# Kernel tuning notes

Measured on AMD Instinct MI355X. Metric: run time of the kernel, lower is better.

The kernel has to match this reference:

```python
import jax, jax.numpy as jnp
import numpy as np

N = 8192
IN_F = 512
OUT_F = 64
ALPHA = 0.2  # LeakyReLU negative slope
NEG_INF = -9e15


def setup_inputs() -> dict:
    key = jax.random.key(0)
    k1, k2, k3, k4 = jax.random.split(key, 4)
    # xavier_uniform-style scale (gain=1.414)
    w_bound = 1.414 * np.sqrt(6.0 / (IN_F + OUT_F))
    a_bound = 1.414 * np.sqrt(6.0 / (2 * OUT_F + 1))
    return {
        "input": jax.random.normal(k1, (N, IN_F), dtype=jnp.float32),
        "adj": jax.random.randint(k2, (N, N), 0, 2, dtype=jnp.int32),
        "W": jax.random.uniform(k3, (IN_F, OUT_F), jnp.float32, -w_bound, w_bound),
        "a": jax.random.uniform(k4, (2 * OUT_F, 1), jnp.float32, -a_bound, a_bound),
        "sig_sample_size": 512,
    }


def reference(input, adj, W, a, sig_sample_size):
    h = input @ W  # [N, F]
    # Split 'a' so e_ij = leakyrelu(a1.h_i + a2.h_j) without the N*N*2F repeat/cat
    a1, a2 = a[:OUT_F, 0], a[OUT_F:, 0]  # [F], [F]
    e = jax.nn.leaky_relu((h @ a1)[:, None] + (h @ a2)[None, :], negative_slope=ALPHA)  # [N, N]
    attention = jnp.where(adj > 0, e, NEG_INF)
    attention = jax.nn.softmax(attention, axis=1)
    sig_scores = jnp.sum(attention, axis=0)  # [N]
    _, indices = jax.lax.top_k(sig_scores, sig_sample_size)
    return indices
```

## Files before the change

kernel.cpp:

```cpp
#include <hip/hip_runtime.h>
#include <stdint.h>

#define NROW 8192
#define IN_F 512
#define OUT_F 64
#define ALPHA 0.2f

__device__ float g_wa1[IN_F];
__device__ float g_wa2[IN_F];
__device__ float g_f1[NROW];
__device__ float g_f2[NROW];
__device__ float g_zinv[NROW];
__device__ double g_colsum[NROW];
__device__ unsigned long long g_mask[(size_t)NROW * 128];

__global__ void prep_wa(const float* __restrict__ W, const float* __restrict__ a) {
    int k = threadIdx.x;
    if (k < IN_F) {
        double s1 = 0.0, s2 = 0.0;
        for (int t = 0; t < OUT_F; ++t) {
            double w = (double)W[k * OUT_F + t];
            s1 += w * (double)a[t];
            s2 += w * (double)a[OUT_F + t];
        }
        g_wa1[k] = (float)s1;
        g_wa2[k] = (float)s2;
        #pragma unroll
        for (int i = 0; i < 16; ++i) g_colsum[k * 16 + i] = 0.0;
    }
}

__global__ void __launch_bounds__(256) compute_f(const float* __restrict__ in) {
    int wave = threadIdx.x >> 6, lane = threadIdx.x & 63;
    int row = blockIdx.x * 4 + wave;
    const float4* in4  = (const float4*)(in + (size_t)row * IN_F);
    const float4* wa14 = (const float4*)g_wa1;
    const float4* wa24 = (const float4*)g_wa2;
    double s1 = 0.0, s2 = 0.0;
    #pragma unroll
    for (int half = 0; half < 2; ++half) {
        int idx = half * 64 + lane;
        float4 x = in4[idx];
        float4 u = wa14[idx];
        float4 v = wa24[idx];
        s1 += (double)x.x*u.x + (double)x.y*u.y + (double)x.z*u.z + (double)x.w*u.w;
        s2 += (double)x.x*v.x + (double)x.y*v.y + (double)x.z*v.z + (double)x.w*v.w;
    }
    #pragma unroll
    for (int off = 32; off > 0; off >>= 1) {
        s1 += __shfl_down(s1, off, 64);
        s2 += __shfl_down(s2, off, 64);
    }
    if (lane == 0) { g_f1[row] = (float)s1; g_f2[row] = (float)s2; }
}

__global__ void __launch_bounds__(256) row_z_mask(const int* __restrict__ adj) {
    __shared__ float f2s[NROW];
    __shared__ double zpart[16];
    int tid = threadIdx.x;
    int wave = tid >> 6, lane = tid & 63;
    for (int k = tid; k < NROW / 4; k += 256)
        ((float4*)f2s)[k] = ((const float4*)g_f2)[k];
    __syncthreads();
    int row0 = blockIdx.x * 4;
    for (int r = 0; r < 4; ++r) {
        int row = row0 + r;
        float f1r = g_f1[row];
        const int4* arow = (const int4*)(adj + (size_t)row * NROW) + wave * 512;
        unsigned long long myword = 0;
        double zacc = 0.0;
        #pragma unroll
        for (int it = 0; it < 8; ++it) {
            int4 av = arow[it * 64 + lane];
            int colbase = wave * 2048 + it * 256 + lane * 4;
            float4 f2v = *(const float4*)&f2s[colbase];
            bool p0 = av.x > 0, p1 = av.y > 0, p2 = av.z > 0, p3 = av.w > 0;
            unsigned long long b0 = __ballot(p0), b1 = __ballot(p1);
            unsigned long long b2 = __ballot(p2), b3 = __ballot(p3);
            int bl = it * 4;
            if (lane == bl)     myword = b0;
            if (lane == bl + 1) myword = b1;
            if (lane == bl + 2) myword = b2;
            if (lane == bl + 3) myword = b3;
            float e0 = f1r + f2v.x; e0 = e0 > 0.f ? e0 : ALPHA * e0;
            float e1 = f1r + f2v.y; e1 = e1 > 0.f ? e1 : ALPHA * e1;
            float e2 = f1r + f2v.z; e2 = e2 > 0.f ? e2 : ALPHA * e2;
            float e3 = f1r + f2v.w; e3 = e3 > 0.f ? e3 : ALPHA * e3;
            zacc += p0 ? (double)expf(e0) : 0.0;
            zacc += p1 ? (double)expf(e1) : 0.0;
            zacc += p2 ? (double)expf(e2) : 0.0;
            zacc += p3 ? (double)expf(e3) : 0.0;
        }
        if (lane < 32) g_mask[(size_t)row * 128 + wave * 32 + lane] = myword;
        #pragma unroll
        for (int off = 32; off > 0; off >>= 1) zacc += __shfl_down(zacc, off, 64);
        if (lane == 0) zpart[r * 4 + wave] = zacc;
    }
    __syncthreads();
    if (tid < 4) {
        double z = zpart[tid*4+0] + zpart[tid*4+1] + zpart[tid*4+2] + zpart[tid*4+3];
        g_zinv[row0 + tid] = (float)(1.0 / z);
    }
}

__global__ void __launch_bounds__(256) colsum_kernel() {
    int tid = threadIdx.x;
    int cb = blockIdx.x & 31;
    int rb = blockIdx.x >> 5;
    int j = cb * 256 + tid;
    float f2j = g_f2[j];
    int wsel = cb * 4 + (tid & 3);
    int bit = (tid >> 2) & 63;
    double acc = 0.0;
    int i0 = rb * 256;
    for (int i = i0; i < i0 + 256; ++i) {
        unsigned long long wv = g_mask[(size_t)i * 128 + wsel];
        float e = g_f1[i] + f2j;
        e = e > 0.f ? e : ALPHA * e;
        float val = expf(e) * g_zinv[i];
        acc += ((wv >> bit) & 1ULL) ? (double)val : 0.0;
    }
    atomicAdd(&g_colsum[j], acc);
}

__global__ void __launch_bounds__(1024) topk_kernel(int* __restrict__ out, int K) {
    __shared__ unsigned int sbits[NROW];
    __shared__ unsigned int hist[256];
    __shared__ unsigned long long cand[1024];
    __shared__ unsigned long long s_prefix;
    __shared__ unsigned int s_want, s_cnt;
    int tid = threadIdx.x;
    for (int k = tid; k < NROW; k += 1024) {
        float s = (float)g_colsum[k];
        unsigned int u = __float_as_uint(s);
        u = (u & 0x80000000u) ? ~u : (u | 0x80000000u);
        sbits[k] = u;
    }
    if (tid == 0) { s_prefix = 0ULL; s_want = (unsigned)K; s_cnt = 0; }
    __syncthreads();
    for (int lvl = 0; lvl < 6; ++lvl) {
        int shift = 40 - lvl * 8;
        if (tid < 256) hist[tid] = 0;
        __syncthreads();
        unsigned long long pmask = (lvl == 0) ? 0ULL : (~0ULL << (shift + 8));
        unsigned long long prefix = s_prefix;
        for (int k = tid; k < NROW; k += 1024) {
            unsigned long long kk =
                ((unsigned long long)sbits[k] << 13) | (unsigned long long)(8191 - k);
            if ((kk & pmask) == prefix)
                atomicAdd(&hist[(unsigned)(kk >> shift) & 255u], 1u);
        }
        __syncthreads();
        if (tid == 0) {
            unsigned cum = 0; int b = 255;
            for (; b >= 0; --b) { cum += hist[b]; if (cum >= s_want) break; }
            if (b < 0) b = 0;
            s_want -= (cum - hist[b]);
            s_prefix |= ((unsigned long long)b << shift);
        }
        __syncthreads();
    }
    unsigned long long thr = s_prefix;
    for (int k = tid; k < NROW; k += 1024) {
        unsigned long long kk =
            ((unsigned long long)sbits[k] << 13) | (unsigned long long)(8191 - k);
        if (kk >= thr) {
            unsigned pos = atomicAdd(&s_cnt, 1u);
            if (pos < 1024u) cand[pos] = kk;
        }
    }
    __syncthreads();
    unsigned cnt = s_cnt;
    if ((unsigned)tid >= cnt) cand[tid] = 0ULL;
    __syncthreads();
    for (int k2 = 2; k2 <= 1024; k2 <<= 1) {
        for (int jj = k2 >> 1; jj > 0; jj >>= 1) {
            int ixj = tid ^ jj;
            if (ixj > tid) {
                unsigned long long a = cand[tid], b = cand[ixj];
                bool up = ((tid & k2) == 0);
                if (up ? (a < b) : (a > b)) { cand[tid] = b; cand[ixj] = a; }
            }
            __syncthreads();
        }
    }
    if (tid < K) out[tid] = 8191 - (int)(cand[tid] & 0x1FFFULL);
}

extern "C" void kernel_launch(void* const* d_in, const int* in_sizes, int n_in,
                              void* d_out, int out_size, void* d_ws, size_t ws_size,
                              hipStream_t stream) {
    const float* input = (const float*)d_in[0];
    const int*   adj   = (const int*)d_in[1];
    const float* W     = (const float*)d_in[2];
    const float* a     = (const float*)d_in[3];
    int* out = (int*)d_out;
    int K = out_size;

    prep_wa<<<1, 512, 0, stream>>>(W, a);
    compute_f<<<NROW / 4, 256, 0, stream>>>(input);
    row_z_mask<<<NROW / 4, 256, 0, stream>>>(adj);
    colsum_kernel<<<1024, 256, 0, stream>>>();
    topk_kernel<<<1, 1024, 0, stream>>>(out, K);
}
```

Baseline: 559.0 us.

## Factor exp(leakyrelu) into separable row and column terms to remove per-pair exp

Uses exp(leakyrelu(f1+f2)) = exp(f1)exp(f2) or exp(0.2 f1)exp(0.2 f2), depending on sign, so the per-element exponentials in both the row-normalizer and column-sum kernels become precomputed per-row and per-column factors. It also stages mask words and row factors in shared memory in the colsum kernel and adds a small kernel that builds the normalized row factors. This trades the N^2 expf calls for extra double-precision accumulators and comparisons. Factoring in exp(f1) and exp(f2) separately can overflow or lose precision, which could shift the top-k ranking.

```diff
diff --git a/kernel.cpp b/kernel.cpp
--- a/kernel.cpp
+++ b/kernel.cpp
@@ -6,11 +6,18 @@
 #define OUT_F 64
 #define ALPHA 0.2f
 
-__device__ float g_wa1[IN_F];
-__device__ float g_wa2[IN_F];
-__device__ float g_f1[NROW];
-__device__ float g_f2[NROW];
-__device__ float g_zinv[NROW];
+__device__ float  g_wa1[IN_F];
+__device__ float  g_wa2[IN_F];
+__device__ float  g_f1[NROW];
+__device__ float  g_f2[NROW];
+__device__ float  g_E2f[NROW];
+__device__ float  g_F2f[NROW];
+__device__ double g_E2d[NROW];
+__device__ double g_F2d[NROW];
+__device__ double g_accp[NROW];
+__device__ double g_accn[NROW];
+__device__ double g_G1[NROW];
+__device__ double g_H1[NROW];
 __device__ double g_colsum[NROW];
 __device__ unsigned long long g_mask[(size_t)NROW * 128];
 
@@ -51,29 +58,40 @@
         s1 += __shfl_down(s1, off, 64);
         s2 += __shfl_down(s2, off, 64);
     }
-    if (lane == 0) { g_f1[row] = (float)s1; g_f2[row] = (float)s2; }
+    if (lane == 0) {
+        float f1 = (float)s1, f2 = (float)s2;
+        g_f1[row] = f1; g_f2[row] = f2;
+        double e2 = exp((double)f2), g2 = exp(0.2 * (double)f2);
+        g_E2d[row] = e2;        g_F2d[row] = g2;
+        g_E2f[row] = (float)e2; g_F2f[row] = (float)g2;
+    }
 }
 
 __global__ void __launch_bounds__(256) row_z_mask(const int* __restrict__ adj) {
-    __shared__ float f2s[NROW];
-    __shared__ double zpart[16];
+    __shared__ float E2s[NROW];
+    __shared__ float F2s[NROW];
+    __shared__ double zp[16], zn[16];
     int tid = threadIdx.x;
     int wave = tid >> 6, lane = tid & 63;
-    for (int k = tid; k < NROW / 4; k += 256)
-        ((float4*)f2s)[k] = ((const float4*)g_f2)[k];
+    for (int k = tid; k < NROW / 4; k += 256) {
+        ((float4*)E2s)[k] = ((const float4*)g_E2f)[k];
+        ((float4*)F2s)[k] = ((const float4*)g_F2f)[k];
+    }
     __syncthreads();
     int row0 = blockIdx.x * 4;
     for (int r = 0; r < 4; ++r) {
         int row = row0 + r;
         float f1r = g_f1[row];
+        float Ft = expf(-0.2f * f1r);
         const int4* arow = (const int4*)(adj + (size_t)row * NROW) + wave * 512;
         unsigned long long myword = 0;
-        double zacc = 0.0;
+        double accp = 0.0, accn = 0.0;
         #pragma unroll
         for (int it = 0; it < 8; ++it) {
             int4 av = arow[it * 64 + lane];
             int colbase = wave * 2048 + it * 256 + lane * 4;
-            float4 f2v = *(const float4*)&f2s[colbase];
+            float4 E2v = *(const float4*)&E2s[colbase];
+            float4 F2v = *(const float4*)&F2s[colbase];
             bool p0 = av.x > 0, p1 = av.y > 0, p2 = av.z > 0, p3 = av.w > 0;
             unsigned long long b0 = __ballot(p0), b1 = __ballot(p1);
             unsigned long long b2 = __ballot(p2), b3 = __ballot(p3);
@@ -82,45 +100,69 @@
             if (lane == bl + 1) myword = b1;
             if (lane == bl + 2) myword = b2;
             if (lane == bl + 3) myword = b3;
-            float e0 = f1r + f2v.x; e0 = e0 > 0.f ? e0 : ALPHA * e0;
-            float e1 = f1r + f2v.y; e1 = e1 > 0.f ? e1 : ALPHA * e1;
-            float e2 = f1r + f2v.z; e2 = e2 > 0.f ? e2 : ALPHA * e2;
-            float e3 = f1r + f2v.w; e3 = e3 > 0.f ? e3 : ALPHA * e3;
-            zacc += p0 ? (double)expf(e0) : 0.0;
-            zacc += p1 ? (double)expf(e1) : 0.0;
-            zacc += p2 ? (double)expf(e2) : 0.0;
-            zacc += p3 ? (double)expf(e3) : 0.0;
+            bool q0 = F2v.x > Ft, q1 = F2v.y > Ft, q2 = F2v.z > Ft, q3 = F2v.w > Ft;
+            accp += (p0 && q0) ? (double)E2v.x : 0.0;
+            accn += (p0 && !q0) ? (double)F2v.x : 0.0;
+            accp += (p1 && q1) ? (double)E2v.y : 0.0;
+            accn += (p1 && !q1) ? (double)F2v.y : 0.0;
+            accp += (p2 && q2) ? (double)E2v.z : 0.0;
+            accn += (p2 && !q2) ? (double)F2v.z : 0.0;
+            accp += (p3 && q3) ? (double)E2v.w : 0.0;
+            accn += (p3 && !q3) ? (double)F2v.w : 0.0;
         }
         if (lane < 32) g_mask[(size_t)row * 128 + wave * 32 + lane] = myword;
         #pragma unroll
-        for (int off = 32; off > 0; off >>= 1) zacc += __shfl_down(zacc, off, 64);
-        if (lane == 0) zpart[r * 4 + wave] = zacc;
+        for (int off = 32; off > 0; off >>= 1) {
+            accp += __shfl_down(accp, off, 64);
+            accn += __shfl_down(accn, off, 64);
+        }
+        if (lane == 0) { zp[r * 4 + wave] = accp; zn[r * 4 + wave] = accn; }
     }
     __syncthreads();
     if (tid < 4) {
-        double z = zpart[tid*4+0] + zpart[tid*4+1] + zpart[tid*4+2] + zpart[tid*4+3];
-        g_zinv[row0 + tid] = (float)(1.0 / z);
-    }
+        g_accp[row0 + tid] = zp[tid*4+0] + zp[tid*4+1] + zp[tid*4+2] + zp[tid*4+3];
+        g_accn[row0 + tid] = zn[tid*4+0] + zn[tid*4+1] + zn[tid*4+2] + zn[tid*4+3];
+    }
+}
+
+__global__ void __launch_bounds__(256) prep_gh() {
+    int i = blockIdx.x * 256 + threadIdx.x;
+    double f1d = (double)g_f1[i];
+    double e1 = exp(f1d), h1 = exp(0.2 * f1d);
+    double Z = e1 * g_accp[i] + h1 * g_accn[i];
+    double zinv = 1.0 / Z;
+    g_G1[i] = e1 * zinv;
+    g_H1[i] = h1 * zinv;
 }
 
 __global__ void __launch_bounds__(256) colsum_kernel() {
+    __shared__ float  f1s[256];
+    __shared__ double G1s[256], H1s[256];
+    __shared__ unsigned long long msk[1024];
     int tid = threadIdx.x;
     int cb = blockIdx.x & 31;
     int rb = blockIdx.x >> 5;
     int j = cb * 256 + tid;
     float f2j = g_f2[j];
-    int wsel = cb * 4 + (tid & 3);
-    int bit = (tid >> 2) & 63;
-    double acc = 0.0;
     int i0 = rb * 256;
-    for (int i = i0; i < i0 + 256; ++i) {
-        unsigned long long wv = g_mask[(size_t)i * 128 + wsel];
-        float e = g_f1[i] + f2j;
-        e = e > 0.f ? e : ALPHA * e;
-        float val = expf(e) * g_zinv[i];
-        acc += ((wv >> bit) & 1ULL) ? (double)val : 0.0;
-    }
-    atomicAdd(&g_colsum[j], acc);
+    f1s[tid] = g_f1[i0 + tid];
+    G1s[tid] = g_G1[i0 + tid];
+    H1s[tid] = g_H1[i0 + tid];
+    for (int t = tid; t < 1024; t += 256)
+        msk[t] = g_mask[(size_t)(i0 + (t >> 2)) * 128 + cb * 4 + (t & 3)];
+    __syncthreads();
+    int c = tid & 3, bit = (tid >> 2) & 63;
+    double accp = 0.0, accn = 0.0;
+    for (int i = 0; i < 256; ++i) {
+        unsigned long long wv = msk[i * 4 + c];
+        bool b = (wv >> bit) & 1ULL;
+        float e = f1s[i] + f2j;
+        bool pos = e > 0.0f;
+        accp += (b && pos)  ? G1s[i] : 0.0;
+        accn += (b && !pos) ? H1s[i] : 0.0;
+    }
+    double res = g_E2d[j] * accp + g_F2d[j] * accn;
+    atomicAdd(&g_colsum[j], res);
 }
 
 __global__ void __launch_bounds__(1024) topk_kernel(int* __restrict__ out, int K) {
@@ -200,6 +242,7 @@
     prep_wa<<<1, 512, 0, stream>>>(W, a);
     compute_f<<<NROW / 4, 256, 0, stream>>>(input);
     row_z_mask<<<NROW / 4, 256, 0, stream>>>(adj);
+    prep_gh<<<NROW / 256, 256, 0, stream>>>();
     colsum_kernel<<<1024, 256, 0, stream>>>();
     topk_kernel<<<1, 1024, 0, stream>>>(out, K);
 }
```

Measured after the change: 513.4 us. 8.1% less time.
